# Kernel tuning notes

Measured on AMD Instinct MI355X. Metric: run time of the kernel, lower is better.

## Reference

```python
import jax, jax.numpy as jnp
import numpy as np

N_NODES = 2048
N_EDGES = 32768
N_IN = 256
MSG_HID = 512
MSG_OUT = 256
N_HID = 512


def _linear_params(key, fan_in, fan_out):
    kw, kb = jax.random.split(key)
    bound = 1.0 / np.sqrt(fan_in)
    W = jax.random.uniform(kw, (fan_out, fan_in), jnp.float32, -bound, bound)
    b = jax.random.uniform(kb, (fan_out,), jnp.float32, -bound, bound)
    return W, b


def setup_inputs() -> dict:
    key = jax.random.key(0)
    ks = jax.random.split(key, 8)
    inputs = jax.random.normal(ks[0], (N_NODES, N_IN), jnp.float32)
    # one-hot incidence matrices built from random receiver/sender node indices
    recv_idx = jax.random.randint(ks[1], (N_EDGES,), 0, N_NODES)
    send_idx = jax.random.randint(ks[2], (N_EDGES,), 0, N_NODES)
    rel_rec = jax.nn.one_hot(recv_idx, N_NODES, dtype=jnp.float32)   # [E, N]
    rel_send = jax.nn.one_hot(send_idx, N_NODES, dtype=jnp.float32)  # [E, N]
    msg_W1, msg_b1 = _linear_params(ks[3], 2 * N_IN, MSG_HID)
    msg_W2, msg_b2 = _linear_params(ks[4], MSG_HID, MSG_OUT)
    out_W1, out_b1 = _linear_params(ks[5], N_IN + MSG_OUT, N_HID)
    out_W2, out_b2 = _linear_params(ks[6], N_HID, N_HID)
    out_W3, out_b3 = _linear_params(ks[7], N_HID, N_IN)
    return {
        'inputs': inputs, 'rel_rec': rel_rec, 'rel_send': rel_send,
        'msg_W1': msg_W1, 'msg_b1': msg_b1, 'msg_W2': msg_W2, 'msg_b2': msg_b2,
        'out_W1': out_W1, 'out_b1': out_b1, 'out_W2': out_W2, 'out_b2': out_b2,
        'out_W3': out_W3, 'out_b3': out_b3,
    }


def reference(inputs, rel_rec, rel_send, msg_W1, msg_b1, msg_W2, msg_b2,
              out_W1, out_b1, out_W2, out_b2, out_W3, out_b3):
    # gather node features to edges via dense one-hot matmuls (as in original)
    receivers = rel_rec @ inputs    # [E, n_in]
    senders = rel_send @ inputs     # [E, n_in]
    pre_msg = jnp.concatenate([senders, receivers], axis=1)  # [E, 2*n_in]
    # edge-message MLP (dropout p=0 -> identity)
    msg = jax.nn.relu(pre_msg @ msg_W1.T + msg_b1)
    msg = jax.nn.relu(msg @ msg_W2.T + msg_b2)               # [E, msg_out]
    # scatter-add messages to receiving nodes: (msg^T @ rel_rec)^T == rel_rec^T @ msg
    agg_msgs = rel_rec.T @ msg                               # [N, msg_out]
    aug_inputs = jnp.concatenate([inputs, agg_msgs], axis=-1)
    # node-update MLP
    pred = jax.nn.relu(aug_inputs @ out_W1.T + out_b1)
    pred = jax.nn.relu(pred @ out_W2.T + out_b2)
    pred = pred @ out_W3.T + out_b3
    return inputs + pred
```

## Files before the change

kernel.cpp:

```cpp
#include <hip/hip_runtime.h>
#include <hip/hip_bf16.h>
#include <stdint.h>

using bf16 = __hip_bfloat16;
typedef short bf16x8 __attribute__((ext_vector_type(8)));
typedef float floatx4 __attribute__((ext_vector_type(4)));

static constexpr int NODES = 2048;
static constexpr int EDGES = 32768;

__device__ inline uint4 cvt8(const float* __restrict__ p) {
    const float4* f = (const float4*)p;
    float4 a = f[0], b = f[1];
    union { uint4 u; bf16 h[8]; } pk;
    pk.h[0] = __float2bfloat16(a.x); pk.h[1] = __float2bfloat16(a.y);
    pk.h[2] = __float2bfloat16(a.z); pk.h[3] = __float2bfloat16(a.w);
    pk.h[4] = __float2bfloat16(b.x); pk.h[5] = __float2bfloat16(b.y);
    pk.h[6] = __float2bfloat16(b.z); pk.h[7] = __float2bfloat16(b.w);
    return pk.u;
}

template<int BM, int BN, int AMODE, int BMODE, int EPI>
__device__ __forceinline__ void gemm_body(
    const bf16* __restrict__ A, const float* __restrict__ Af,
    const float* __restrict__ Bt, const float* __restrict__ bias,
    bf16* __restrict__ Cout, float* __restrict__ OutF,
    const float* __restrict__ inputsF, const bf16* __restrict__ UVb,
    const float* __restrict__ b1v, const int* __restrict__ sidx,
    const int* __restrict__ ridx, const float* __restrict__ aggin,
    float* __restrict__ aggout, int M, int N, int K, int bx, int by)
{
    constexpr int BK = 32;
    constexpr int PA = BM / 64;
    constexpr int PB = BN / 64;
    constexpr int MI = BM / 32;
    constexpr int NJ = BN / 32;
    __shared__ bf16 As[BM * BK];
    __shared__ bf16 Bs[BN * BK];
    __shared__ int sIdx[BM];
    __shared__ int rIdx[BM];

    const int t = threadIdx.x;
    const int m0 = by * BM;
    const int n0 = bx * BN;

    if constexpr (AMODE == 3) {
        if (t < BM) {
            sIdx[t] = sidx[m0 + t] & (NODES - 1);
            rIdx[t] = ridx[m0 + t] & (NODES - 1);
        }
        __syncthreads();
    }

    const int sr = t >> 2;
    const int sc = t & 3;

    uint4 ra[PA], rb[PB];

    auto loadTiles = [&](int kt) {
        const int kk = kt * BK + sc * 8;
#pragma unroll
        for (int p = 0; p < PA; ++p) {
            const int row = p * 64 + sr;
            if constexpr (AMODE == 0) {
                ra[p] = *(const uint4*)(A + (size_t)(m0 + row) * K + kk);
            } else if constexpr (AMODE == 1) {
                ra[p] = cvt8(Af + (size_t)(m0 + row) * K + kk);
            } else if constexpr (AMODE == 2) {
                const float* src = (kk < 256)
                    ? (inputsF + (size_t)(m0 + row) * 256 + kk)
                    : (aggin + (size_t)(m0 + row) * 256 + (kk - 256));
                ra[p] = cvt8(src);
            } else {
                union { uint4 q; unsigned short h[8]; } uu, vv;
                uu.q = *(const uint4*)(UVb + (size_t)sIdx[row] * 1024 + kk);
                vv.q = *(const uint4*)(UVb + (size_t)rIdx[row] * 1024 + 512 + kk);
                const float4* c = (const float4*)(b1v + kk);
                float4 c0 = c[0], c1 = c[1];
                const float cf[8] = {c0.x, c0.y, c0.z, c0.w, c1.x, c1.y, c1.z, c1.w};
                union { uint4 q; bf16 h[8]; } pk;
#pragma unroll
                for (int e = 0; e < 8; ++e) {
                    union { unsigned int u; float f; } a2, b2;
                    a2.u = (unsigned int)uu.h[e] << 16;
                    b2.u = (unsigned int)vv.h[e] << 16;
                    pk.h[e] = __float2bfloat16(fmaxf(a2.f + b2.f + cf[e], 0.f));
                }
                ra[p] = pk.q;
            }
        }
#pragma unroll
        for (int p = 0; p < PB; ++p) {
            const int row = p * 64 + sr;
            if constexpr (BMODE == 0) {
                rb[p] = cvt8(Bt + (size_t)(n0 + row) * K + kk);
            } else {
                const int n = n0 + row;
                rb[p] = cvt8(Bt + (size_t)(n & 511) * 512 + (n >> 9) * 256 + kk);
            }
        }
    };

    const int wv = t >> 6;
    const int lane = t & 63;
    const int wm = wv >> 1, wn = wv & 1;
    const int r16 = lane & 15, q = lane >> 4;

    floatx4 acc[MI][NJ] = {};

    loadTiles(0);
    const int KT = K / BK;
    for (int kt = 0; kt < KT; ++kt) {
        __syncthreads();
#pragma unroll
        for (int p = 0; p < PA; ++p)
            *(uint4*)(&As[(p * 64 + sr) * BK + sc * 8]) = ra[p];
#pragma unroll
        for (int p = 0; p < PB; ++p)
            *(uint4*)(&Bs[(p * 64 + sr) * BK + sc * 8]) = rb[p];
        __syncthreads();
        if (kt + 1 < KT) loadTiles(kt + 1);

        bf16x8 af[MI], bfr[NJ];
#pragma unroll
        for (int i = 0; i < MI; ++i)
            af[i] = *(const bf16x8*)(&As[(wm * (BM / 2) + i * 16 + r16) * BK + q * 8]);
#pragma unroll
        for (int j = 0; j < NJ; ++j)
            bfr[j] = *(const bf16x8*)(&Bs[(wn * (BN / 2) + j * 16 + r16) * BK + q * 8]);
#pragma unroll
        for (int i = 0; i < MI; ++i)
#pragma unroll
            for (int j = 0; j < NJ; ++j)
                acc[i][j] = __builtin_amdgcn_mfma_f32_16x16x32_bf16(af[i], bfr[j], acc[i][j], 0, 0, 0);
    }

    float bv[NJ];
#pragma unroll
    for (int j = 0; j < NJ; ++j)
        bv[j] = (EPI == 3 || EPI == 4) ? 0.f : bias[n0 + wn * (BN / 2) + j * 16 + r16];

#pragma unroll
    for (int i = 0; i < MI; ++i) {
        const int lr = wm * (BM / 2) + i * 16 + q * 4;
        const int rbase = m0 + lr;
#pragma unroll
        for (int j = 0; j < NJ; ++j) {
            const int gc = n0 + wn * (BN / 2) + j * 16 + r16;
#pragma unroll
            for (int r = 0; r < 4; ++r) {
                float v = acc[i][j][r] + bv[j];
                const int gr = rbase + r;
                if constexpr (EPI == 0) {
                    v = fmaxf(v, 0.0f);
                    Cout[(size_t)gr * N + gc] = __float2bfloat16(v);
                } else if constexpr (EPI == 1) {
                    v = fmaxf(v, 0.0f);
                    atomicAdd(&aggout[(size_t)rIdx[lr + r] * 256 + gc], v);
                } else if constexpr (EPI == 2) {
                    OutF[(size_t)gr * 256 + gc] = inputsF[(size_t)gr * 256 + gc] + v;
                } else if constexpr (EPI == 3) {
                    OutF[(size_t)gr * N + gc] = v;
                } else {
                    Cout[(size_t)gr * N + gc] = __float2bfloat16(v);
                }
            }
        }
    }
}

template<int BM, int BN, int AMODE, int BMODE, int EPI>
__global__ __launch_bounds__(256, 2) void gemm_k(
    const bf16* __restrict__ A, const float* __restrict__ Af,
    const float* __restrict__ Bt, const float* __restrict__ bias,
    bf16* __restrict__ Cout, float* __restrict__ OutF,
    const float* __restrict__ inputsF, const bf16* __restrict__ UVb,
    const float* __restrict__ b1v, const int* __restrict__ sidx,
    const int* __restrict__ ridx, const float* __restrict__ aggin,
    float* __restrict__ aggout, int M, int N, int K)
{
    gemm_body<BM, BN, AMODE, BMODE, EPI>(A, Af, Bt, bias, Cout, OutF, inputsF,
        UVb, b1v, sidx, ridx, aggin, aggout, M, N, K, blockIdx.x, blockIdx.y);
}

__global__ __launch_bounds__(256, 8) void fat_pre(
    const float* __restrict__ rel_rec, const float* __restrict__ rel_send,
    int* __restrict__ recv_idx, int* __restrict__ send_idx,
    float4* __restrict__ agg, const float* __restrict__ inputs,
    const float* __restrict__ msg_W1, bf16* __restrict__ UVb)
{
    const int b = blockIdx.x;
    if (b < 512) {
        gemm_body<64, 64, 1, 1, 4>(nullptr, inputs, msg_W1, nullptr, UVb, nullptr,
            nullptr, nullptr, nullptr, nullptr, nullptr, nullptr, nullptr,
            NODES, 1024, 256, b & 15, b >> 4);
    } else if (b < 1024) {
        agg[(size_t)(b - 512) * 256 + threadIdx.x] = float4{0.f, 0.f, 0.f, 0.f};
    } else {
        const int eb = b - 1024;
        const int half = eb >> 13;
        const int rb = eb & 8191;
        const float* mat = half ? rel_send : rel_rec;
        int* out = half ? send_idx : recv_idx;
        const int w = threadIdx.x >> 6;
        const int lane = threadIdx.x & 63;
        const int row = rb * 4 + w;
        if (lane == 0) out[row] = 0;
        const uint4* base = (const uint4*)(mat + (size_t)row * NODES);
        for (int p = 0; p < 8; ++p) {
            uint4 v = base[p * 64 + lane];
            const bool hit = (v.x | v.y | v.z | v.w) != 0u;
            if (hit) {
                int e = v.x ? 0 : (v.y ? 1 : (v.z ? 2 : 3));
                out[row] = p * 256 + lane * 4 + e;
            }
            if (__any(hit)) break;
        }
    }
}

extern "C" void kernel_launch(void* const* d_in, const int* in_sizes, int n_in,
                              void* d_out, int out_size, void* d_ws, size_t ws_size,
                              hipStream_t stream) {
    const float* inputs   = (const float*)d_in[0];
    const float* rel_rec  = (const float*)d_in[1];
    const float* rel_send = (const float*)d_in[2];
    const float* msg_W1   = (const float*)d_in[3];
    const float* msg_b1   = (const float*)d_in[4];
    const float* msg_W2   = (const float*)d_in[5];
    const float* msg_b2   = (const float*)d_in[6];
    const float* out_W1   = (const float*)d_in[7];
    const float* out_b1   = (const float*)d_in[8];
    const float* out_W2   = (const float*)d_in[9];
    const float* out_b2   = (const float*)d_in[10];
    const float* out_W3   = (const float*)d_in[11];
    const float* out_b3   = (const float*)d_in[12];

    char* ws = (char*)d_ws;
    int*   recv_idx = (int*)(ws + 0);
    int*   send_idx = (int*)(ws + 131072);
    float* agg      = (float*)(ws + 262144);
    bf16*  UVb      = (bf16*)(ws + 2359296);
    bf16*  g1       = (bf16*)(ws + 6553600);
    bf16*  g2       = (bf16*)(ws + 8650752);
    if (ws_size < (size_t)11 * 1024 * 1024) return;

    fat_pre<<<17408, 256, 0, stream>>>(rel_rec, rel_send, recv_idx, send_idx,
                                       (float4*)agg, inputs, msg_W1, UVb);

    gemm_k<128, 128, 3, 0, 1><<<dim3(2, 256), 256, 0, stream>>>(
        nullptr, nullptr, msg_W2, msg_b2, nullptr, nullptr,
        nullptr, UVb, msg_b1, send_idx, recv_idx, nullptr, agg,
        EDGES, 256, 512);

    gemm_k<64, 64, 2, 0, 0><<<dim3(8, 32), 256, 0, stream>>>(
        nullptr, nullptr, out_W1, out_b1, g1, nullptr,
        inputs, nullptr, nullptr, nullptr, nullptr, agg, nullptr,
        NODES, 512, 512);

    gemm_k<64, 64, 0, 0, 0><<<dim3(8, 32), 256, 0, stream>>>(
        g1, nullptr, out_W2, out_b2, g2, nullptr,
        nullptr, nullptr, nullptr, nullptr, nullptr, nullptr, nullptr,
        NODES, 512, 512);

    gemm_k<64, 64, 0, 0, 2><<<dim3(4, 32), 256, 0, stream>>>(
        g2, nullptr, out_W3, out_b3, nullptr, (float*)d_out,
        inputs, nullptr, nullptr, nullptr, nullptr, nullptr, nullptr,
        NODES, 256, 512);
}
```

Before: 594.2 us.

## Fuse pipeline into persistent megakernel with software grid barriers

Replaces the five separate launches with a small zeroing kernel plus one persistent 768-block kernel whose stages are separated by atomic-counter grid barriers. All GEMMs move to a single 64x256 tile shape. The one-hot index extraction is spread across all blocks, including those that also run the UV GEMM. This removes launch gaps and inter-kernel drains, but much of the grid idles in the later stages, the edge GEMM gets fewer, larger tiles, and the grid barrier deadlocks if not all 768 blocks are co-resident.

New measurement: 919.5 us. +54.7%, slower.

```diff
diff --git a/kernel.cpp b/kernel.cpp
--- a/kernel.cpp
+++ b/kernel.cpp
@@ -8,6 +8,7 @@
 
 static constexpr int NODES = 2048;
 static constexpr int EDGES = 32768;
+static constexpr int GRID  = 768;
 
 __device__ inline uint4 cvt8(const float* __restrict__ p) {
     const float4* f = (const float4*)p;
@@ -20,26 +21,32 @@
     return pk.u;
 }
 
-template<int BM, int BN, int AMODE, int BMODE, int EPI>
-__device__ __forceinline__ void gemm_body(
+__device__ __forceinline__ void gridbar(int* __restrict__ bar, int target) {
+    __syncthreads();
+    if (threadIdx.x == 0) {
+        __threadfence();
+        atomicAdd(bar, 1);
+        while (__hip_atomic_load(bar, __ATOMIC_RELAXED, __HIP_MEMORY_SCOPE_AGENT) < target)
+            __builtin_amdgcn_s_sleep(8);
+        __threadfence();
+    }
+    __syncthreads();
+}
+
+template<int AMODE, int BMODE, int EPI>
+__device__ __forceinline__ void gemm64x256(
     const bf16* __restrict__ A, const float* __restrict__ Af,
     const float* __restrict__ Bt, const float* __restrict__ bias,
     bf16* __restrict__ Cout, float* __restrict__ OutF,
     const float* __restrict__ inputsF, const bf16* __restrict__ UVb,
     const float* __restrict__ b1v, const int* __restrict__ sidx,
     const int* __restrict__ ridx, const float* __restrict__ aggin,
-    float* __restrict__ aggout, int M, int N, int K, int bx, int by)
+    float* __restrict__ aggout, int M, int N, int K, int bx, int by,
+    bf16* __restrict__ As, bf16* __restrict__ Bs,
+    int* __restrict__ sIdx, int* __restrict__ rIdx)
 {
-    constexpr int BK = 32;
-    constexpr int PA = BM / 64;
-    constexpr int PB = BN / 64;
-    constexpr int MI = BM / 32;
-    constexpr int NJ = BN / 32;
-    __shared__ bf16 As[BM * BK];
-    __shared__ bf16 Bs[BN * BK];
-    __shared__ int sIdx[BM];
-    __shared__ int rIdx[BM];
-
+    constexpr int BM = 64, BN = 256, BK = 32;
+    constexpr int PB = 4, MI = 2, NJ = 8;
     const int t = threadIdx.x;
     const int m0 = by * BM;
     const int n0 = bx * BN;
@@ -49,45 +56,41 @@
             sIdx[t] = sidx[m0 + t] & (NODES - 1);
             rIdx[t] = ridx[m0 + t] & (NODES - 1);
         }
-        __syncthreads();
-    }
+    }
+    __syncthreads();
 
     const int sr = t >> 2;
     const int sc = t & 3;
 
-    uint4 ra[PA], rb[PB];
+    uint4 ra, rb[PB];
 
     auto loadTiles = [&](int kt) {
         const int kk = kt * BK + sc * 8;
-#pragma unroll
-        for (int p = 0; p < PA; ++p) {
-            const int row = p * 64 + sr;
-            if constexpr (AMODE == 0) {
-                ra[p] = *(const uint4*)(A + (size_t)(m0 + row) * K + kk);
-            } else if constexpr (AMODE == 1) {
-                ra[p] = cvt8(Af + (size_t)(m0 + row) * K + kk);
-            } else if constexpr (AMODE == 2) {
-                const float* src = (kk < 256)
-                    ? (inputsF + (size_t)(m0 + row) * 256 + kk)
-                    : (aggin + (size_t)(m0 + row) * 256 + (kk - 256));
-                ra[p] = cvt8(src);
-            } else {
-                union { uint4 q; unsigned short h[8]; } uu, vv;
-                uu.q = *(const uint4*)(UVb + (size_t)sIdx[row] * 1024 + kk);
-                vv.q = *(const uint4*)(UVb + (size_t)rIdx[row] * 1024 + 512 + kk);
-                const float4* c = (const float4*)(b1v + kk);
-                float4 c0 = c[0], c1 = c[1];
-                const float cf[8] = {c0.x, c0.y, c0.z, c0.w, c1.x, c1.y, c1.z, c1.w};
-                union { uint4 q; bf16 h[8]; } pk;
-#pragma unroll
-                for (int e = 0; e < 8; ++e) {
-                    union { unsigned int u; float f; } a2, b2;
-                    a2.u = (unsigned int)uu.h[e] << 16;
-                    b2.u = (unsigned int)vv.h[e] << 16;
-                    pk.h[e] = __float2bfloat16(fmaxf(a2.f + b2.f + cf[e], 0.f));
-                }
-                ra[p] = pk.q;
-            }
+        if constexpr (AMODE == 0) {
+            ra = *(const uint4*)(A + (size_t)(m0 + sr) * K + kk);
+        } else if constexpr (AMODE == 1) {
+            ra = cvt8(Af + (size_t)(m0 + sr) * K + kk);
+        } else if constexpr (AMODE == 2) {
+            const float* src = (kk < 256)
+                ? (inputsF + (size_t)(m0 + sr) * 256 + kk)
+                : (aggin + (size_t)(m0 + sr) * 256 + (kk - 256));
+            ra = cvt8(src);
+        } else {
+            union { uint4 q; unsigned short h[8]; } uu, vv;
+            uu.q = *(const uint4*)(UVb + (size_t)sIdx[sr] * 1024 + kk);
+            vv.q = *(const uint4*)(UVb + (size_t)rIdx[sr] * 1024 + 512 + kk);
+            const float4* c = (const float4*)(b1v + kk);
+            float4 c0 = c[0], c1 = c[1];
+            const float cf[8] = {c0.x, c0.y, c0.z, c0.w, c1.x, c1.y, c1.z, c1.w};
+            union { uint4 q; bf16 h[8]; } pk;
+#pragma unroll
+            for (int e = 0; e < 8; ++e) {
+                union { unsigned int u; float f; } a2, b2;
+                a2.u = (unsigned int)uu.h[e] << 16;
+                b2.u = (unsigned int)vv.h[e] << 16;
+                pk.h[e] = __float2bfloat16(fmaxf(a2.f + b2.f + cf[e], 0.f));
+            }
+            ra = pk.q;
         }
 #pragma unroll
         for (int p = 0; p < PB; ++p) {
@@ -112,9 +115,7 @@
     const int KT = K / BK;
     for (int kt = 0; kt < KT; ++kt) {
         __syncthreads();
-#pragma unroll
-        for (int p = 0; p < PA; ++p)
-            *(uint4*)(&As[(p * 64 + sr) * BK + sc * 8]) = ra[p];
+        *(uint4*)(&As[sr * BK + sc * 8]) = ra;
 #pragma unroll
         for (int p = 0; p < PB; ++p)
             *(uint4*)(&Bs[(p * 64 + sr) * BK + sc * 8]) = rb[p];
@@ -124,10 +125,10 @@
         bf16x8 af[MI], bfr[NJ];
 #pragma unroll
         for (int i = 0; i < MI; ++i)
-            af[i] = *(const bf16x8*)(&As[(wm * (BM / 2) + i * 16 + r16) * BK + q * 8]);
+            af[i] = *(const bf16x8*)(&As[(wm * 32 + i * 16 + r16) * BK + q * 8]);
 #pragma unroll
         for (int j = 0; j < NJ; ++j)
-            bfr[j] = *(const bf16x8*)(&Bs[(wn * (BN / 2) + j * 16 + r16) * BK + q * 8]);
+            bfr[j] = *(const bf16x8*)(&Bs[(wn * 128 + j * 16 + r16) * BK + q * 8]);
 #pragma unroll
         for (int i = 0; i < MI; ++i)
 #pragma unroll
@@ -138,15 +139,15 @@
     float bv[NJ];
 #pragma unroll
     for (int j = 0; j < NJ; ++j)
-        bv[j] = (EPI == 3 || EPI == 4) ? 0.f : bias[n0 + wn * (BN / 2) + j * 16 + r16];
+        bv[j] = (EPI == 4) ? 0.f : bias[n0 + wn * 128 + j * 16 + r16];
 
 #pragma unroll
     for (int i = 0; i < MI; ++i) {
-        const int lr = wm * (BM / 2) + i * 16 + q * 4;
+        const int lr = wm * 32 + i * 16 + q * 4;
         const int rbase = m0 + lr;
 #pragma unroll
         for (int j = 0; j < NJ; ++j) {
-            const int gc = n0 + wn * (BN / 2) + j * 16 + r16;
+            const int gc = n0 + wn * 128 + j * 16 + r16;
 #pragma unroll
             for (int r = 0; r < 4; ++r) {
                 float v = acc[i][j][r] + bv[j];
@@ -159,64 +160,95 @@
                     atomicAdd(&aggout[(size_t)rIdx[lr + r] * 256 + gc], v);
                 } else if constexpr (EPI == 2) {
                     OutF[(size_t)gr * 256 + gc] = inputsF[(size_t)gr * 256 + gc] + v;
-                } else if constexpr (EPI == 3) {
-                    OutF[(size_t)gr * N + gc] = v;
                 } else {
                     Cout[(size_t)gr * N + gc] = __float2bfloat16(v);
                 }
             }
         }
     }
-}
-
-template<int BM, int BN, int AMODE, int BMODE, int EPI>
-__global__ __launch_bounds__(256, 2) void gemm_k(
-    const bf16* __restrict__ A, const float* __restrict__ Af,
-    const float* __restrict__ Bt, const float* __restrict__ bias,
-    bf16* __restrict__ Cout, float* __restrict__ OutF,
-    const float* __restrict__ inputsF, const bf16* __restrict__ UVb,
-    const float* __restrict__ b1v, const int* __restrict__ sidx,
-    const int* __restrict__ ridx, const float* __restrict__ aggin,
-    float* __restrict__ aggout, int M, int N, int K)
+    __syncthreads();
+}
+
+__global__ __launch_bounds__(256) void zero_pre(float4* __restrict__ agg,
+                                                int* __restrict__ bar) {
+    if (blockIdx.x < 512) {
+        agg[(size_t)blockIdx.x * 256 + threadIdx.x] = float4{0.f, 0.f, 0.f, 0.f};
+    } else if (threadIdx.x == 0) {
+        *bar = 0;
+    }
+}
+
+__global__ __launch_bounds__(256, 4) void mega(
+    const float* __restrict__ inputs, const float* __restrict__ rel_rec,
+    const float* __restrict__ rel_send, const float* __restrict__ msg_W1,
+    const float* __restrict__ msg_b1, const float* __restrict__ msg_W2,
+    const float* __restrict__ msg_b2, const float* __restrict__ out_W1,
+    const float* __restrict__ out_b1, const float* __restrict__ out_W2,
+    const float* __restrict__ out_b2, const float* __restrict__ out_W3,
+    const float* __restrict__ out_b3, int* __restrict__ recv_idx,
+    int* __restrict__ send_idx, float* __restrict__ agg,
+    bf16* __restrict__ UVb, bf16* __restrict__ g1, bf16* __restrict__ g2,
+    int* __restrict__ bar, float* __restrict__ outF)
 {
-    gemm_body<BM, BN, AMODE, BMODE, EPI>(A, Af, Bt, bias, Cout, OutF, inputsF,
-        UVb, b1v, sidx, ridx, aggin, aggout, M, N, K, blockIdx.x, blockIdx.y);
-}
-
-__global__ __launch_bounds__(256, 8) void fat_pre(
-    const float* __restrict__ rel_rec, const float* __restrict__ rel_send,
-    int* __restrict__ recv_idx, int* __restrict__ send_idx,
-    float4* __restrict__ agg, const float* __restrict__ inputs,
-    const float* __restrict__ msg_W1, bf16* __restrict__ UVb)
-{
+    __shared__ bf16 As[64 * 32];
+    __shared__ bf16 Bs[256 * 32];
+    __shared__ int sIdx[64];
+    __shared__ int rIdx[64];
     const int b = blockIdx.x;
-    if (b < 512) {
-        gemm_body<64, 64, 1, 1, 4>(nullptr, inputs, msg_W1, nullptr, UVb, nullptr,
+    const int t = threadIdx.x;
+
+    if (b < 128)
+        gemm64x256<1, 1, 4>(nullptr, inputs, msg_W1, nullptr, UVb, nullptr,
             nullptr, nullptr, nullptr, nullptr, nullptr, nullptr, nullptr,
-            NODES, 1024, 256, b & 15, b >> 4);
-    } else if (b < 1024) {
-        agg[(size_t)(b - 512) * 256 + threadIdx.x] = float4{0.f, 0.f, 0.f, 0.f};
-    } else {
-        const int eb = b - 1024;
-        const int half = eb >> 13;
-        const int rb = eb & 8191;
-        const float* mat = half ? rel_send : rel_rec;
-        int* out = half ? send_idx : recv_idx;
-        const int w = threadIdx.x >> 6;
-        const int lane = threadIdx.x & 63;
-        const int row = rb * 4 + w;
-        if (lane == 0) out[row] = 0;
-        const uint4* base = (const uint4*)(mat + (size_t)row * NODES);
-        for (int p = 0; p < 8; ++p) {
-            uint4 v = base[p * 64 + lane];
-            const bool hit = (v.x | v.y | v.z | v.w) != 0u;
-            if (hit) {
-                int e = v.x ? 0 : (v.y ? 1 : (v.z ? 2 : 3));
-                out[row] = p * 256 + lane * 4 + e;
-            }
-            if (__any(hit)) break;
-        }
-    }
+            NODES, 1024, 256, b & 3, b >> 2, As, Bs, sIdx, rIdx);
+    {
+        const int w = t >> 6, lane = t & 63;
+        int base, cnt;
+        if (b < 128) { base = (b * 4 + w) * 8;                cnt = 8;  }
+        else         { base = 4096 + ((b - 128) * 4 + w) * 24; cnt = 24; }
+        for (int i = 0; i < cnt; ++i) {
+            const int x = base + i;
+            const int half = x >> 15;
+            const int row = x & 32767;
+            const float* mat = half ? rel_send : rel_rec;
+            int* out = half ? send_idx : recv_idx;
+            if (lane == 0) out[row] = 0;
+            const uint4* bp = (const uint4*)(mat + (size_t)row * NODES);
+            for (int p = 0; p < 8; ++p) {
+                uint4 v = bp[p * 64 + lane];
+                const bool hit = (v.x | v.y | v.z | v.w) != 0u;
+                if (hit) {
+                    int e = v.x ? 0 : (v.y ? 1 : (v.z ? 2 : 3));
+                    out[row] = p * 256 + lane * 4 + e;
+                }
+                if (__any(hit)) break;
+            }
+        }
+    }
+    gridbar(bar, GRID * 1);
+
+    if (b < 512)
+        gemm64x256<3, 0, 1>(nullptr, nullptr, msg_W2, msg_b2, nullptr, nullptr,
+            nullptr, UVb, msg_b1, send_idx, recv_idx, nullptr, agg,
+            EDGES, 256, 512, 0, b, As, Bs, sIdx, rIdx);
+    gridbar(bar, GRID * 2);
+
+    if (b < 64)
+        gemm64x256<2, 0, 0>(nullptr, nullptr, out_W1, out_b1, g1, nullptr,
+            inputs, nullptr, nullptr, nullptr, nullptr, agg, nullptr,
+            NODES, 512, 512, b & 1, b >> 1, As, Bs, sIdx, rIdx);
+    gridbar(bar, GRID * 3);
+
+    if (b < 64)
+        gemm64x256<0, 0, 0>(g1, nullptr, out_W2, out_b2, g2, nullptr,
+            nullptr, nullptr, nullptr, nullptr, nullptr, nullptr, nullptr,
+            NODES, 512, 512, b & 1, b >> 1, As, Bs, sIdx, rIdx);
+    gridbar(bar, GRID * 4);
+
+    if (b < 32)
+        gemm64x256<0, 0, 2>(g2, nullptr, out_W3, out_b3, nullptr, outF,
+            inputs, nullptr, nullptr, nullptr, nullptr, nullptr, nullptr,
+            NODES, 256, 512, 0, b, As, Bs, sIdx, rIdx);
 }
 
 extern "C" void kernel_launch(void* const* d_in, const int* in_sizes, int n_in,
@@ -243,28 +275,12 @@
     bf16*  UVb      = (bf16*)(ws + 2359296);
     bf16*  g1       = (bf16*)(ws + 6553600);
     bf16*  g2       = (bf16*)(ws + 8650752);
+    int*   bar      = (int*)(ws + 10747904);
     if (ws_size < (size_t)11 * 1024 * 1024) return;
 
-    fat_pre<<<17408, 256, 0, stream>>>(rel_rec, rel_send, recv_idx, send_idx,
-                                       (float4*)agg, inputs, msg_W1, UVb);
-
-    gemm_k<128, 128, 3, 0, 1><<<dim3(2, 256), 256, 0, stream>>>(
-        nullptr, nullptr, msg_W2, msg_b2, nullptr, nullptr,
-        nullptr, UVb, msg_b1, send_idx, recv_idx, nullptr, agg,
-        EDGES, 256, 512);
-
-    gemm_k<64, 64, 2, 0, 0><<<dim3(8, 32), 256, 0, stream>>>(
-        nullptr, nullptr, out_W1, out_b1, g1, nullptr,
-        inputs, nullptr, nullptr, nullptr, nullptr, agg, nullptr,
-        NODES, 512, 512);
-
-    gemm_k<64, 64, 0, 0, 0><<<dim3(8, 32), 256, 0, stream>>>(
-        g1, nullptr, out_W2, out_b2, g2, nullptr,
-        nullptr, nullptr, nullptr, nullptr, nullptr, nullptr, nullptr,
-        NODES, 512, 512);
-
-    gemm_k<64, 64, 0, 0, 2><<<dim3(4, 32), 256, 0, stream>>>(
-        g2, nullptr, out_W3, out_b3, nullptr, (float*)d_out,
-        inputs, nullptr, nullptr, nullptr, nullptr, nullptr, nullptr,
-        NODES, 256, 512);
-}
+    zero_pre<<<513, 256, 0, stream>>>((float4*)agg, bar);
+
+    mega<<<GRID, 256, 0, stream>>>(inputs, rel_rec, rel_send, msg_W1, msg_b1,
+        msg_W2, msg_b2, out_W1, out_b1, out_W2, out_b2, out_W3, out_b3,
+        recv_idx, send_idx, agg, UVb, g1, g2, bar, (float*)d_out);
+}
```

## Fuse three node-MLP GEMM launches into one kernel with grid barriers

Applied to the files above, without the earlier changes.

Replaces the three separate node-update GEMM launches with a single persistent kernel of 256 blocks that runs all three layers, separated by software grid-wide barriers built on an atomic counter. The counter is reset inside the preceding kernel. The aim is to remove two kernel launch gaps and their tail effects. The cost is spin-wait synchronization, plus a reliance on all 256 blocks being co-resident, which the launch bounds should allow on this GPU. The unused EPI==3 path is also removed.

Result: slower. 622.4 us (+4.7%).

```diff
diff --git a/kernel.cpp b/kernel.cpp
--- a/kernel.cpp
+++ b/kernel.cpp
@@ -18,6 +18,18 @@
     pk.h[4] = __float2bfloat16(b.x); pk.h[5] = __float2bfloat16(b.y);
     pk.h[6] = __float2bfloat16(b.z); pk.h[7] = __float2bfloat16(b.w);
     return pk.u;
+}
+
+__device__ __forceinline__ void gridbar(int* __restrict__ bar, int target) {
+    __syncthreads();
+    if (threadIdx.x == 0) {
+        __threadfence();
+        atomicAdd(bar, 1);
+        while (__hip_atomic_load(bar, __ATOMIC_RELAXED, __HIP_MEMORY_SCOPE_AGENT) < target)
+            __builtin_amdgcn_s_sleep(8);
+        __threadfence();
+    }
+    __syncthreads();
 }
 
 template<int BM, int BN, int AMODE, int BMODE, int EPI>
@@ -138,7 +150,7 @@
     float bv[NJ];
 #pragma unroll
     for (int j = 0; j < NJ; ++j)
-        bv[j] = (EPI == 3 || EPI == 4) ? 0.f : bias[n0 + wn * (BN / 2) + j * 16 + r16];
+        bv[j] = (EPI == 4) ? 0.f : bias[n0 + wn * (BN / 2) + j * 16 + r16];
 
 #pragma unroll
     for (int i = 0; i < MI; ++i) {
@@ -159,8 +171,6 @@
                     atomicAdd(&aggout[(size_t)rIdx[lr + r] * 256 + gc], v);
                 } else if constexpr (EPI == 2) {
                     OutF[(size_t)gr * 256 + gc] = inputsF[(size_t)gr * 256 + gc] + v;
-                } else if constexpr (EPI == 3) {
-                    OutF[(size_t)gr * N + gc] = v;
                 } else {
                     Cout[(size_t)gr * N + gc] = __float2bfloat16(v);
                 }
@@ -187,7 +197,8 @@
     const float* __restrict__ rel_rec, const float* __restrict__ rel_send,
     int* __restrict__ recv_idx, int* __restrict__ send_idx,
     float4* __restrict__ agg, const float* __restrict__ inputs,
-    const float* __restrict__ msg_W1, bf16* __restrict__ UVb)
+    const float* __restrict__ msg_W1, bf16* __restrict__ UVb,
+    int* __restrict__ bar)
 {
     const int b = blockIdx.x;
     if (b < 512) {
@@ -195,6 +206,7 @@
             nullptr, nullptr, nullptr, nullptr, nullptr, nullptr, nullptr,
             NODES, 1024, 256, b & 15, b >> 4);
     } else if (b < 1024) {
+        if (b == 512 && threadIdx.x == 0) *bar = 0;
         agg[(size_t)(b - 512) * 256 + threadIdx.x] = float4{0.f, 0.f, 0.f, 0.f};
     } else {
         const int eb = b - 1024;
@@ -219,6 +231,29 @@
     }
 }
 
+__global__ __launch_bounds__(256, 2) void node_mlp(
+    const float* __restrict__ inputs, const float* __restrict__ out_W1,
+    const float* __restrict__ out_b1, const float* __restrict__ out_W2,
+    const float* __restrict__ out_b2, const float* __restrict__ out_W3,
+    const float* __restrict__ out_b3, const float* __restrict__ agg,
+    bf16* __restrict__ g1, bf16* __restrict__ g2, float* __restrict__ outF,
+    int* __restrict__ bar)
+{
+    const int b = blockIdx.x;
+    gemm_body<64, 64, 2, 0, 0>(nullptr, nullptr, out_W1, out_b1, g1, nullptr,
+        inputs, nullptr, nullptr, nullptr, nullptr, agg, nullptr,
+        NODES, 512, 512, b & 7, b >> 3);
+    gridbar(bar, 256);
+    gemm_body<64, 64, 0, 0, 0>(g1, nullptr, out_W2, out_b2, g2, nullptr,
+        nullptr, nullptr, nullptr, nullptr, nullptr, nullptr, nullptr,
+        NODES, 512, 512, b & 7, b >> 3);
+    gridbar(bar, 512);
+    if (b < 128)
+        gemm_body<64, 64, 0, 0, 2>(g2, nullptr, out_W3, out_b3, nullptr, outF,
+            inputs, nullptr, nullptr, nullptr, nullptr, nullptr, nullptr,
+            NODES, 256, 512, b & 3, b >> 2);
+}
+
 extern "C" void kernel_launch(void* const* d_in, const int* in_sizes, int n_in,
                               void* d_out, int out_size, void* d_ws, size_t ws_size,
                               hipStream_t stream) {
@@ -243,28 +278,17 @@
     bf16*  UVb      = (bf16*)(ws + 2359296);
     bf16*  g1       = (bf16*)(ws + 6553600);
     bf16*  g2       = (bf16*)(ws + 8650752);
+    int*   bar      = (int*)(ws + 10747904);
     if (ws_size < (size_t)11 * 1024 * 1024) return;
 
     fat_pre<<<17408, 256, 0, stream>>>(rel_rec, rel_send, recv_idx, send_idx,
-                                       (float4*)agg, inputs, msg_W1, UVb);
+                                       (float4*)agg, inputs, msg_W1, UVb, bar);
 
     gemm_k<128, 128, 3, 0, 1><<<dim3(2, 256), 256, 0, stream>>>(
         nullptr, nullptr, msg_W2, msg_b2, nullptr, nullptr,
         nullptr, UVb, msg_b1, send_idx, recv_idx, nullptr, agg,
         EDGES, 256, 512);
 
-    gemm_k<64, 64, 2, 0, 0><<<dim3(8, 32), 256, 0, stream>>>(
-        nullptr, nullptr, out_W1, out_b1, g1, nullptr,
-        inputs, nullptr, nullptr, nullptr, nullptr, agg, nullptr,
-        NODES, 512, 512);
-
-    gemm_k<64, 64, 0, 0, 0><<<dim3(8, 32), 256, 0, stream>>>(
-        g1, nullptr, out_W2, out_b2, g2, nullptr,
-        nullptr, nullptr, nullptr, nullptr, nullptr, nullptr, nullptr,
-        NODES, 512, 512);
-
-    gemm_k<64, 64, 0, 0, 2><<<dim3(4, 32), 256, 0, stream>>>(
-        g2, nullptr, out_W3, out_b3, nullptr, (float*)d_out,
-        inputs, nullptr, nullptr, nullptr, nullptr, nullptr, nullptr,
-        NODES, 256, 512);
-}
+    node_mlp<<<256, 256, 0, stream>>>(inputs, out_W1, out_b1, out_W2, out_b2,
+        out_W3, out_b3, agg, g1, g2, (float*)d_out, bar);
+}
```
